# Kernel optimization log

Measured on AMD Instinct MI355X. Metric: run time of the kernel, lower is better.

## Reference

```python
import jax, jax.numpy as jnp
import numpy as np

B, S, D = 4, 2048, 1024
DFF = 4096        # dense FFN hidden
E, DFE = 8, 1024  # n_experts, expert hidden
K = 2             # top-k routing
LAM = 0.5         # coe_lambda


def setup_inputs() -> dict:
    key = jax.random.key(0)
    ks = jax.random.split(key, 10)
    s = 0.02
    return {
        "x":   jax.random.normal(ks[0], (B, S, D), jnp.float32),
        "W1":  jax.random.normal(ks[1], (D, DFF), jnp.float32) * s,
        "b1":  jnp.zeros((DFF,), jnp.float32),
        "W2":  jax.random.normal(ks[2], (DFF, D), jnp.float32) * s,
        "b2":  jnp.zeros((D,), jnp.float32),
        "Wg":  jax.random.normal(ks[3], (D, E), jnp.float32) * s,
        "We1": jax.random.normal(ks[4], (E, D, DFE), jnp.float32) * s,
        "be1": jnp.zeros((E, DFE), jnp.float32),
        "We2": jax.random.normal(ks[5], (E, DFE, D), jnp.float32) * s,
        "be2": jnp.zeros((E, D), jnp.float32),
        "id":  S // 2,  # python int cutoff: tokens < id are FFN-only
    }


def reference(x, W1, b1, W2, b2, Wg, We1, be1, We2, be2, id):
    # Dense FFN applied to every token (both branches compute it).
    ffn_out = jax.nn.gelu(x @ W1 + b1) @ W2 + b2                   # [B,S,D]

    # MoE: softmax router, top-k renormalized gates.
    probs = jax.nn.softmax(x @ Wg, axis=-1)                        # [B,S,E]
    topv, topi = jax.lax.top_k(probs, K)                           # [B,S,K]
    topv = topv / topv.sum(-1, keepdims=True)
    gates = (jax.nn.one_hot(topi, E, dtype=x.dtype) * topv[..., None]).sum(-2)  # [B,S,E]

    # All-expert dense evaluation, then gated combine.
    h = jax.nn.gelu(jnp.einsum('bsd,edf->bsef', x, We1) + be1)     # [B,S,E,DFE]
    eo = jnp.einsum('bsef,efd->bsed', h, We2) + be2                # [B,S,E,D]
    moe_out = jnp.einsum('bse,bsed->bsd', gates, eo)               # [B,S,D]

    # Branch selection: token i < id (and S != 1) -> FFN only; else FFN + lam*MoE.
    seq = x.shape[1]
    mask = ((jnp.arange(seq) >= id) | (seq == 1)).astype(x.dtype)  # [S]
    return ffn_out + LAM * mask[None, :, None] * moe_out
```

## Files before the change

### kernel.cpp

```cpp
#include <hip/hip_runtime.h>
#include <hip/hip_bf16.h>
#include <cstdint>
#include <cstddef>

typedef unsigned short ushort_t;
typedef __bf16 bf16x8v __attribute__((ext_vector_type(8)));
typedef float f32x4 __attribute__((ext_vector_type(4)));

#define Bsz 4
#define Sseq 2048
#define Dd 1024
#define DFFd 4096
#define Ee 8
#define DFEd 1024
#define IDCUT 1024
#define NTOK (Bsz*Sseq)
#define NMOE (Bsz*(Sseq-IDCUT))
#define MAXSLOT 4096

__device__ __forceinline__ ushort_t f2bf(float f) {
  unsigned u = __float_as_uint(f);
  u += 0x7fffu + ((u >> 16) & 1u);
  return (ushort_t)(u >> 16);
}

__device__ __forceinline__ unsigned pk2bf(float a, float b) {
  return (unsigned)f2bf(a) | ((unsigned)f2bf(b) << 16);
}

__device__ __forceinline__ float gelu_f(float x) {
  float u = x * (1.0f + 0.044715f * x * x);
  float s = 1.0f / (1.0f + __expf(-1.5957691216057308f * u));
  return x * s;
}

__device__ __forceinline__ void gload_lds16(const void* g, void* l) {
  __builtin_amdgcn_global_load_lds(
      (const __attribute__((address_space(1))) void*)g,
      (__attribute__((address_space(3))) void*)l,
      16, 0, 0);
}

__global__ __launch_bounds__(256) void cast_k(
    const float* __restrict__ x, ushort_t* __restrict__ xb)
{
  const int row  = blockIdx.x * 4 + (threadIdx.x >> 6);
  const int lane = threadIdx.x & 63;
  const float* xr = x + (size_t)row * Dd;
  ushort_t* xbr = xb + (size_t)row * Dd;
  float4 v[4];
  #pragma unroll
  for (int j = 0; j < 4; ++j) v[j] = ((const float4*)xr)[lane + j * 64];
  #pragma unroll
  for (int j = 0; j < 4; ++j) {
    ushort4 o;
    o.x = f2bf(v[j].x); o.y = f2bf(v[j].y); o.z = f2bf(v[j].z); o.w = f2bf(v[j].w);
    ((ushort4*)xbr)[lane + j * 64] = o;
  }
}

__global__ __launch_bounds__(256) void router_k(
    const float* __restrict__ x, const float* __restrict__ Wg,
    int* __restrict__ cnt, int* __restrict__ slots, float* __restrict__ gsv)
{
  __shared__ int   eTok[128];
  __shared__ int   lbase[8];
  const int wid = threadIdx.x >> 6, lane = threadIdx.x & 63;
  const int tblk = blockIdx.x * 64;

  #pragma unroll 1
  for (int it = 0; it < 16; ++it) {
    const int ti = it * 4 + wid;
    const int t  = tblk + ti;
    const int b  = t >> 10, s = (t & 1023) + IDCUT;
    const float* xr = x + ((size_t)b * Sseq + s) * Dd;
    float4 accA = {0.f,0.f,0.f,0.f}, accB = {0.f,0.f,0.f,0.f};
    #pragma unroll
    for (int j = 0; j < 4; ++j) {
      const float4 v = ((const float4*)xr)[lane + j * 64];
      const int kbase = (lane + j * 64) * 4;
      #pragma unroll
      for (int r = 0; r < 4; ++r) {
        const float xv = (r == 0) ? v.x : (r == 1) ? v.y : (r == 2) ? v.z : v.w;
        const float4 wa = *(const float4*)(Wg + (size_t)(kbase + r) * 8);
        const float4 wb = *(const float4*)(Wg + (size_t)(kbase + r) * 8 + 4);
        accA.x += xv * wa.x; accA.y += xv * wa.y; accA.z += xv * wa.z; accA.w += xv * wa.w;
        accB.x += xv * wb.x; accB.y += xv * wb.y; accB.z += xv * wb.z; accB.w += xv * wb.w;
      }
    }
    float acc[8] = {accA.x, accA.y, accA.z, accA.w, accB.x, accB.y, accB.z, accB.w};
    #pragma unroll
    for (int off = 32; off > 0; off >>= 1) {
      #pragma unroll
      for (int e8 = 0; e8 < 8; ++e8) acc[e8] += __shfl_xor(acc[e8], off);
    }
    if (lane == 0) {
      int e0 = 0; float v0 = acc[0];
      #pragma unroll
      for (int e8 = 1; e8 < 8; ++e8) if (acc[e8] > v0) { v0 = acc[e8]; e0 = e8; }
      int e1 = -1; float v1 = -3.4e38f;
      #pragma unroll
      for (int e8 = 0; e8 < 8; ++e8) if (e8 != e0 && acc[e8] > v1) { v1 = acc[e8]; e1 = e8; }
      float g0 = 1.0f / (1.0f + expf(v1 - v0));
      eTok[ti * 2] = e0; eTok[ti * 2 + 1] = e1;
      gsv[t * 2] = g0;  gsv[t * 2 + 1] = 1.0f - g0;
    }
  }
  __syncthreads();
  if (wid == 0) {
    int cnts[8] = {0,0,0,0,0,0,0,0};
    int el[2];
    #pragma unroll
    for (int p = 0; p < 2; ++p) {
      el[p] = eTok[p * 64 + lane];
      #pragma unroll
      for (int e = 0; e < 8; ++e)
        cnts[e] += __popcll(__ballot(el[p] == e));
    }
    if (lane < 8) lbase[lane] = atomicAdd(&cnt[lane], cnts[lane]);
    int run[8];
    #pragma unroll
    for (int e = 0; e < 8; ++e) run[e] = lbase[e];
    #pragma unroll
    for (int p = 0; p < 2; ++p) {
      const int ent = p * 64 + lane;
      const int val = (tblk + (ent >> 1)) * 2 + (ent & 1);
      #pragma unroll
      for (int e = 0; e < 8; ++e) {
        unsigned long long m = __ballot(el[p] == e);
        if (el[p] == e)
          slots[e * MAXSLOT + run[e] + __popcll(m & ((1ull << lane) - 1ull))] = val;
        run[e] += __popcll(m);
      }
    }
  }
}

__device__ __forceinline__ void t64x128(const float* __restrict__ in,
                                        ushort_t* __restrict__ out,
                                        int R, int C, int by, int bx,
                                        float* __restrict__ lds) {
  const int t = threadIdx.x;
  const int c4 = t & 31;
  const int r0 = t >> 5;
  const float* src = in + (size_t)(by * 64) * C + bx * 128;
  #pragma unroll
  for (int p = 0; p < 8; ++p) {
    const int r = r0 + p * 8;
    const float4 vv = *(const float4*)(src + (size_t)r * C + c4 * 4);
    *(float4*)(lds + r * 129 + c4 * 4) = vv;
  }
  __syncthreads();
  ushort_t* dst = out + (size_t)(bx * 128) * R + by * 64;
  const int rr0 = (t & 7) * 8;
  #pragma unroll
  for (int p = 0; p < 4; ++p) {
    const int cc = (t >> 3) + p * 32;
    const float* col = lds + (size_t)rr0 * 129 + cc;
    float f0 = col[0*129], f1 = col[1*129], f2 = col[2*129], f3 = col[3*129];
    float f4 = col[4*129], f5 = col[5*129], f6 = col[6*129], f7 = col[7*129];
    uint4 q;
    q.x = pk2bf(f0, f1); q.y = pk2bf(f2, f3);
    q.z = pk2bf(f4, f5); q.w = pk2bf(f6, f7);
    *(uint4*)(dst + (size_t)cc * R + rr0) = q;
  }
}

__global__ __launch_bounds__(256) void twcast_k(
    const float* __restrict__ W1, ushort_t* __restrict__ W1t,
    const float* __restrict__ W2, ushort_t* __restrict__ W2t,
    const float* __restrict__ We1, ushort_t* __restrict__ We1t,
    const float* __restrict__ We2, ushort_t* __restrict__ We2t)
{
  __shared__ float lds[64 * 129];
  const int wg = blockIdx.x;
  if (wg < 512) {
    t64x128(W1, W1t, Dd, DFFd, wg >> 5, wg & 31, lds);
  } else if (wg < 1024) {
    const int i = wg - 512;
    t64x128(W2, W2t, DFFd, Dd, i >> 3, i & 7, lds);
  } else if (wg < 2048) {
    const int i = wg - 1024, z = i >> 7, rem = i & 127;
    t64x128(We1 + (size_t)z * Dd * DFEd, We1t + (size_t)z * Dd * DFEd,
            Dd, DFEd, rem >> 3, rem & 7, lds);
  } else {
    const int i = wg - 2048, z = i >> 7, rem = i & 127;
    t64x128(We2 + (size_t)z * DFEd * Dd, We2t + (size_t)z * DFEd * Dd,
            DFEd, Dd, rem >> 3, rem & 7, lds);
  }
}

template<int MODE>
__device__ __forceinline__ void gemm_tile(
    int nt, int mt, int e,
    const ushort_t* __restrict__ A, const ushort_t* __restrict__ Bt,
    const float* __restrict__ biase, void* __restrict__ C,
    int M, int lda, int N, int ldc,
    const int* __restrict__ cnt, const int* __restrict__ slots,
    const float* __restrict__ gates,
    ushort_t* Al, ushort_t* Bl)
{
  int rows = M;
  const int* slist = nullptr;
  if (MODE >= 2) {
    rows = cnt[e];
    if (mt * 128 >= rows) return;
    slist = slots + e * MAXSLOT;
  }
  const ushort_t* Bte = (MODE >= 2) ? (Bt + (size_t)e * (size_t)lda * (size_t)N) : Bt;

  const int tid  = threadIdx.x;
  const int lane = tid & 63;
  const int wid  = tid >> 6;
  const int wr   = wid >> 1, wc = wid & 1;
  const int lr   = lane & 15;
  const int lg   = lane >> 4;
  const int swz7 = lane & 7;

  const ushort_t* gA[4];
  const ushort_t* gB[4];
  #pragma unroll
  for (int j = 0; j < 4; ++j) {
    int tt = j * 256 + tid;
    int rl = tt >> 3, slot = tt & 7;
    int col8 = slot ^ (rl & 7);
    int grow = mt * 128 + rl;
    size_t rowoff;
    if (MODE < 2) {
      rowoff = (size_t)grow;
    } else {
      int idx = grow > rows - 1 ? rows - 1 : grow;
      int sv = slist[idx];
      if (MODE == 2) { int t = sv >> 1; rowoff = (size_t)((t >> 10) * Sseq + IDCUT + (t & 1023)); }
      else           { rowoff = (size_t)sv; }
    }
    gA[j] = A + rowoff * (size_t)lda + col8 * 8;
    gB[j] = Bte + (size_t)(nt * 128 + rl) * (size_t)lda + col8 * 8;
  }

  f32x4 acc[4][4];
  const f32x4 vzero = {0.f, 0.f, 0.f, 0.f};
  #pragma unroll
  for (int m = 0; m < 4; ++m)
    #pragma unroll
    for (int n = 0; n < 4; ++n) acc[m][n] = vzero;

  const unsigned aRow = (unsigned)((wr * 64 + lr) * 128);
  const unsigned bRow = (unsigned)((wc * 64 + lr) * 128);
  const unsigned s0 = (unsigned)((lg ^ swz7) << 4);
  const unsigned s1 = (unsigned)(((4 + lg) ^ swz7) << 4);

  for (int k0 = 0; k0 < lda; k0 += 64) {
    __syncthreads();
    #pragma unroll
    for (int j = 0; j < 4; ++j)
      gload_lds16(gA[j] + k0, (void*)((char*)Al + (j * 256 + wid * 64) * 16));
    #pragma unroll
    for (int j = 0; j < 4; ++j)
      gload_lds16(gB[j] + k0, (void*)((char*)Bl + (j * 256 + wid * 64) * 16));
    __syncthreads();

    {
      bf16x8v af[4], bfr[4];
      #pragma unroll
      for (int mi = 0; mi < 4; ++mi)
        af[mi] = *(const bf16x8v*)((const char*)Al + aRow + mi * 2048 + s0);
      #pragma unroll
      for (int ni = 0; ni < 4; ++ni)
        bfr[ni] = *(const bf16x8v*)((const char*)Bl + bRow + ni * 2048 + s0);
      #pragma unroll
      for (int mi = 0; mi < 4; ++mi)
        #pragma unroll
        for (int ni = 0; ni < 4; ++ni)
          acc[mi][ni] = __builtin_amdgcn_mfma_f32_16x16x32_bf16(
              af[mi], bfr[ni], acc[mi][ni], 0, 0, 0);
    }
    {
      bf16x8v af[4], bfr[4];
      #pragma unroll
      for (int mi = 0; mi < 4; ++mi)
        af[mi] = *(const bf16x8v*)((const char*)Al + aRow + mi * 2048 + s1);
      #pragma unroll
      for (int ni = 0; ni < 4; ++ni)
        bfr[ni] = *(const bf16x8v*)((const char*)Bl + bRow + ni * 2048 + s1);
      #pragma unroll
      for (int mi = 0; mi < 4; ++mi)
        #pragma unroll
        for (int ni = 0; ni < 4; ++ni)
          acc[mi][ni] = __builtin_amdgcn_mfma_f32_16x16x32_bf16(
              af[mi], bfr[ni], acc[mi][ni], 0, 0, 0);
    }
  }

  #pragma unroll
  for (int mf = 0; mf < 4; ++mf) {
    #pragma unroll
    for (int jj = 0; jj < 4; ++jj) {
      const int lrow = wr * 64 + mf * 16 + lg * 4 + jj;
      const int grow = mt * 128 + lrow;
      size_t crow; float gt = 0.f;
      if (MODE >= 2) {
        if (grow >= rows) continue;
        int sv = slist[grow];
        if (MODE == 3) {
          gt = gates[sv];
          int tkn = sv >> 1;
          crow = (size_t)((tkn >> 10) * Sseq + IDCUT + (tkn & 1023));
        } else {
          crow = (size_t)sv;
        }
      } else {
        crow = (size_t)grow;
      }
      #pragma unroll
      for (int nf = 0; nf < 4; ++nf) {
        const int gcol = nt * 128 + wc * 64 + nf * 16 + lr;
        float v = acc[mf][nf][jj] + biase[gcol];
        if (MODE == 0 || MODE == 2) {
          ((ushort_t*)C)[crow * (size_t)ldc + gcol] = f2bf(gelu_f(v));
        } else if (MODE == 1) {
          ((float*)C)[crow * (size_t)ldc + gcol] = v;
        } else {
          atomicAdd(&((float*)C)[crow * (size_t)ldc + gcol], 0.5f * gt * v);
        }
      }
    }
  }
}

__global__ __launch_bounds__(256, 3) void fused1_k(
    const ushort_t* __restrict__ xb,
    const ushort_t* __restrict__ W1t, const float* __restrict__ b1, ushort_t* __restrict__ h1,
    const ushort_t* __restrict__ We1t, const float* __restrict__ be1, ushort_t* __restrict__ hs,
    const int* __restrict__ cnt, const int* __restrict__ slots)
{
  __shared__ ushort_t Al[128 * 64];
  __shared__ ushort_t Bl[128 * 64];
  int wg = blockIdx.x;
  if (wg < 2048) {
    int xcd = wg & 7, idx = wg >> 3;
    int ntB = idx >> 6, mtL = (idx >> 3) & 7, ntS = idx & 7;
    int mt = xcd * 8 + mtL, nt = ntB * 8 + ntS;
    gemm_tile<0>(nt, mt, 0, xb, W1t, b1, (void*)h1, NTOK, Dd, DFFd, DFFd,
                 nullptr, nullptr, nullptr, Al, Bl);
  } else {
    int i = wg - 2048;
    int e = i & 7, j = i >> 3;
    int mt = j >> 3, nt = j & 7;
    gemm_tile<2>(nt, mt, e, xb, We1t, be1 + e * DFEd, (void*)hs, 0, Dd, DFEd, DFEd,
                 cnt, slots, nullptr, Al, Bl);
  }
}

__global__ __launch_bounds__(256, 3) void ffn2_k(
    const ushort_t* __restrict__ h1,
    const ushort_t* __restrict__ W2t, const float* __restrict__ b2,
    float* __restrict__ out)
{
  __shared__ ushort_t Al[128 * 64];
  __shared__ ushort_t Bl[128 * 64];
  int wg = blockIdx.x;
  int xcd = wg & 7, idx = wg >> 3;
  int nt = idx >> 3, mtL = idx & 7;
  int mt = xcd * 8 + mtL;
  gemm_tile<1>(nt, mt, 0, h1, W2t, b2, (void*)out, NTOK, DFFd, Dd, Dd,
               nullptr, nullptr, nullptr, Al, Bl);
}

__global__ __launch_bounds__(256, 3) void moe2_k(
    const ushort_t* __restrict__ hs,
    const ushort_t* __restrict__ We2t, const float* __restrict__ be2,
    float* __restrict__ out,
    const int* __restrict__ cnt, const int* __restrict__ slots,
    const float* __restrict__ gsv)
{
  __shared__ ushort_t Al[128 * 64];
  __shared__ ushort_t Bl[128 * 64];
  int wg = blockIdx.x;
  int e = wg & 7, j = wg >> 3;
  int mt = j >> 3, nt = j & 7;
  gemm_tile<3>(nt, mt, e, hs, We2t, be2 + e * Dd, (void*)out, 0, DFEd, Dd, Dd,
               cnt, slots, gsv, Al, Bl);
}

#define WS_XB    ((size_t)0)
#define WS_W1T   ((size_t)16777216)
#define WS_W2T   ((size_t)25165824)
#define WS_WE1T  ((size_t)33554432)
#define WS_WE2T  ((size_t)50331648)
#define WS_H1    ((size_t)67108864)
#define WS_HS    ((size_t)134217728)
#define WS_CNT   ((size_t)184549376)
#define WS_SLOT  ((size_t)184549632)
#define WS_GSV   ((size_t)184680704)

extern "C" void kernel_launch(void* const* d_in, const int* in_sizes, int n_in,
                              void* d_out, int out_size, void* d_ws, size_t ws_size,
                              hipStream_t stream) {
  const float* x   = (const float*)d_in[0];
  const float* W1  = (const float*)d_in[1];
  const float* b1  = (const float*)d_in[2];
  const float* W2  = (const float*)d_in[3];
  const float* b2  = (const float*)d_in[4];
  const float* Wg  = (const float*)d_in[5];
  const float* We1 = (const float*)d_in[6];
  const float* be1 = (const float*)d_in[7];
  const float* We2 = (const float*)d_in[8];
  const float* be2 = (const float*)d_in[9];
  float* out = (float*)d_out;

  char* ws = (char*)d_ws;
  ushort_t* xb   = (ushort_t*)(ws + WS_XB);
  ushort_t* W1t  = (ushort_t*)(ws + WS_W1T);
  ushort_t* W2t  = (ushort_t*)(ws + WS_W2T);
  ushort_t* We1t = (ushort_t*)(ws + WS_WE1T);
  ushort_t* We2t = (ushort_t*)(ws + WS_WE2T);
  ushort_t* h1   = (ushort_t*)(ws + WS_H1);
  ushort_t* hs   = (ushort_t*)(ws + WS_HS);
  int*      cnt  = (int*)(ws + WS_CNT);
  int*      slots= (int*)(ws + WS_SLOT);
  float*    gsv  = (float*)(ws + WS_GSV);

  hipMemsetAsync(cnt, 0, 8 * sizeof(int), stream);

  cast_k<<<dim3(2048), 256, 0, stream>>>(x, xb);
  router_k<<<dim3(64), 256, 0, stream>>>(x, Wg, cnt, slots, gsv);
  twcast_k<<<dim3(3072), 256, 0, stream>>>(W1, W1t, W2, W2t, We1, We1t, We2, We2t);

  fused1_k<<<dim3(4096), 256, 0, stream>>>(xb, W1t, b1, h1, We1t, be1, hs, cnt, slots);
  ffn2_k<<<dim3(512), 256, 0, stream>>>(h1, W2t, b2, out);
  moe2_k<<<dim3(2048), 256, 0, stream>>>(hs, We2t, be2, out, cnt, slots, gsv);
}
```

Measured before the change: 302.9 us.

## Merge prep kernels and overlap W2/We2 transposes with first GEMM

Folds the x cast, router and W1/We1 transpose-casts into one prep launch, and moves the W2/We2 transpose-casts into the tail of the first GEMM kernel's grid. The aim is to cut launch count and let the second-stage weight conversion overlap with the first-stage GEMM instead of running before it. In exchange, LDS for the GEMM kernel grows to the transpose buffer size (about 33KB), which may lower occupancy under launch_bounds(256,3). The transpose blocks also sit at the end of the grid and compete with GEMM tiles.

```diff
diff --git a/kernel.cpp b/kernel.cpp
--- a/kernel.cpp
+++ b/kernel.cpp
@@ -41,10 +41,9 @@
       16, 0, 0);
 }
 
-__global__ __launch_bounds__(256) void cast_k(
-    const float* __restrict__ x, ushort_t* __restrict__ xb)
-{
-  const int row  = blockIdx.x * 4 + (threadIdx.x >> 6);
+__device__ __forceinline__ void cast_dev(const float* __restrict__ x,
+                                         ushort_t* __restrict__ xb, int wg) {
+  const int row  = wg * 4 + (threadIdx.x >> 6);
   const int lane = threadIdx.x & 63;
   const float* xr = x + (size_t)row * Dd;
   ushort_t* xbr = xb + (size_t)row * Dd;
@@ -59,14 +58,13 @@
   }
 }
 
-__global__ __launch_bounds__(256) void router_k(
+__device__ __forceinline__ void router_dev(
     const float* __restrict__ x, const float* __restrict__ Wg,
-    int* __restrict__ cnt, int* __restrict__ slots, float* __restrict__ gsv)
-{
-  __shared__ int   eTok[128];
-  __shared__ int   lbase[8];
+    int* __restrict__ cnt, int* __restrict__ slots, float* __restrict__ gsv,
+    int blk, int* __restrict__ eTok, int* __restrict__ lbase)
+{
   const int wid = threadIdx.x >> 6, lane = threadIdx.x & 63;
-  const int tblk = blockIdx.x * 64;
+  const int tblk = blk * 64;
 
   #pragma unroll 1
   for (int it = 0; it < 16; ++it) {
@@ -166,27 +164,27 @@
   }
 }
 
-__global__ __launch_bounds__(256) void twcast_k(
+__global__ __launch_bounds__(256) void prep1_k(
+    const float* __restrict__ x, ushort_t* __restrict__ xb,
+    const float* __restrict__ Wg,
+    int* __restrict__ cnt, int* __restrict__ slots, float* __restrict__ gsv,
     const float* __restrict__ W1, ushort_t* __restrict__ W1t,
-    const float* __restrict__ W2, ushort_t* __restrict__ W2t,
-    const float* __restrict__ We1, ushort_t* __restrict__ We1t,
-    const float* __restrict__ We2, ushort_t* __restrict__ We2t)
-{
-  __shared__ float lds[64 * 129];
+    const float* __restrict__ We1, ushort_t* __restrict__ We1t)
+{
+  __shared__ char smemraw[64 * 129 * 4];
   const int wg = blockIdx.x;
-  if (wg < 512) {
-    t64x128(W1, W1t, Dd, DFFd, wg >> 5, wg & 31, lds);
-  } else if (wg < 1024) {
-    const int i = wg - 512;
-    t64x128(W2, W2t, DFFd, Dd, i >> 3, i & 7, lds);
-  } else if (wg < 2048) {
-    const int i = wg - 1024, z = i >> 7, rem = i & 127;
+  if (wg < 2048) {
+    cast_dev(x, xb, wg);
+  } else if (wg < 2112) {
+    router_dev(x, Wg, cnt, slots, gsv, wg - 2048,
+               (int*)smemraw, (int*)(smemraw + 512));
+  } else if (wg < 2624) {
+    const int i = wg - 2112;
+    t64x128(W1, W1t, Dd, DFFd, i >> 5, i & 31, (float*)smemraw);
+  } else {
+    const int i = wg - 2624, z = i >> 7, rem = i & 127;
     t64x128(We1 + (size_t)z * Dd * DFEd, We1t + (size_t)z * Dd * DFEd,
-            Dd, DFEd, rem >> 3, rem & 7, lds);
-  } else {
-    const int i = wg - 2048, z = i >> 7, rem = i & 127;
-    t64x128(We2 + (size_t)z * DFEd * Dd, We2t + (size_t)z * DFEd * Dd,
-            DFEd, Dd, rem >> 3, rem & 7, lds);
+            Dd, DFEd, rem >> 3, rem & 7, (float*)smemraw);
   }
 }
 
@@ -332,10 +330,13 @@
     const ushort_t* __restrict__ xb,
     const ushort_t* __restrict__ W1t, const float* __restrict__ b1, ushort_t* __restrict__ h1,
     const ushort_t* __restrict__ We1t, const float* __restrict__ be1, ushort_t* __restrict__ hs,
-    const int* __restrict__ cnt, const int* __restrict__ slots)
-{
-  __shared__ ushort_t Al[128 * 64];
-  __shared__ ushort_t Bl[128 * 64];
+    const int* __restrict__ cnt, const int* __restrict__ slots,
+    const float* __restrict__ W2, ushort_t* __restrict__ W2t,
+    const float* __restrict__ We2, ushort_t* __restrict__ We2t)
+{
+  __shared__ char smemraw[64 * 129 * 4];
+  ushort_t* Al = (ushort_t*)smemraw;
+  ushort_t* Bl = (ushort_t*)(smemraw + 16384);
   int wg = blockIdx.x;
   if (wg < 2048) {
     int xcd = wg & 7, idx = wg >> 3;
@@ -343,12 +344,19 @@
     int mt = xcd * 8 + mtL, nt = ntB * 8 + ntS;
     gemm_tile<0>(nt, mt, 0, xb, W1t, b1, (void*)h1, NTOK, Dd, DFFd, DFFd,
                  nullptr, nullptr, nullptr, Al, Bl);
-  } else {
+  } else if (wg < 4096) {
     int i = wg - 2048;
     int e = i & 7, j = i >> 3;
     int mt = j >> 3, nt = j & 7;
     gemm_tile<2>(nt, mt, e, xb, We1t, be1 + e * DFEd, (void*)hs, 0, Dd, DFEd, DFEd,
                  cnt, slots, nullptr, Al, Bl);
+  } else if (wg < 4608) {
+    const int i = wg - 4096;
+    t64x128(W2, W2t, DFFd, Dd, i >> 3, i & 7, (float*)smemraw);
+  } else {
+    const int i = wg - 4608, z = i >> 7, rem = i & 127;
+    t64x128(We2 + (size_t)z * DFEd * Dd, We2t + (size_t)z * DFEd * Dd,
+            DFEd, Dd, rem >> 3, rem & 7, (float*)smemraw);
   }
 }
 
@@ -423,11 +431,10 @@
 
   hipMemsetAsync(cnt, 0, 8 * sizeof(int), stream);
 
-  cast_k<<<dim3(2048), 256, 0, stream>>>(x, xb);
-  router_k<<<dim3(64), 256, 0, stream>>>(x, Wg, cnt, slots, gsv);
-  twcast_k<<<dim3(3072), 256, 0, stream>>>(W1, W1t, W2, W2t, We1, We1t, We2, We2t);
-
-  fused1_k<<<dim3(4096), 256, 0, stream>>>(xb, W1t, b1, h1, We1t, be1, hs, cnt, slots);
+  prep1_k<<<dim3(3648), 256, 0, stream>>>(x, xb, Wg, cnt, slots, gsv,
+                                          W1, W1t, We1, We1t);
+  fused1_k<<<dim3(5632), 256, 0, stream>>>(xb, W1t, b1, h1, We1t, be1, hs,
+                                           cnt, slots, W2, W2t, We2, We2t);
   ffn2_k<<<dim3(512), 256, 0, stream>>>(h1, W2t, b2, out);
   moe2_k<<<dim3(2048), 256, 0, stream>>>(hs, We2t, be2, out, cnt, slots, gsv);
 }
```

Result: faster. 292.9 us (-3.3%).
